# Performance work log

Measured on AMD Instinct MI355X. Metric: run time of the kernel, lower is better.

Reference implementation:

```python
import jax, jax.numpy as jnp
import numpy as np
import math

B, T, F, H, C = 512, 26, 2048, 1024, 22


def _lstm_cell(x_t, h, c, Wih, Whh, bih, bhh):
    # PyTorch gate order: i, f, g, o. Gates: [B, 4H]
    gates = x_t @ Wih.T + h @ Whh.T + bih + bhh
    i, f, g, o = jnp.split(gates, 4, axis=-1)
    c_new = jax.nn.sigmoid(f) * c + jax.nn.sigmoid(i) * jnp.tanh(g)
    h_new = jax.nn.sigmoid(o) * jnp.tanh(c_new)
    return h_new, c_new


def setup_inputs() -> dict:
    key = jax.random.key(0)
    ks = jax.random.split(key, 13)
    s_enc = 1.0 / math.sqrt(H)
    inp = {
        "x": jax.random.normal(ks[0], (B, T, F), jnp.float32),
        "enc_Wih": jax.random.normal(ks[1], (4 * H, F), jnp.float32) * s_enc,
        "enc_Whh": jax.random.normal(ks[2], (4 * H, H), jnp.float32) * s_enc,
        "enc_bih": jax.random.normal(ks[3], (4 * H,), jnp.float32) * s_enc,
        "enc_bhh": jax.random.normal(ks[4], (4 * H,), jnp.float32) * s_enc,
        "proj_W": jax.random.normal(ks[5], (H, H), jnp.float32) * s_enc,
        "proj_b": jax.random.normal(ks[6], (H,), jnp.float32) * s_enc,
        "dec_Wih": jax.random.normal(ks[7], (4 * H, H + F), jnp.float32) * s_enc,
        "dec_Whh": jax.random.normal(ks[8], (4 * H, H), jnp.float32) * s_enc,
        "dec_bih": jax.random.normal(ks[9], (4 * H,), jnp.float32) * s_enc,
        "dec_bhh": jax.random.normal(ks[10], (4 * H,), jnp.float32) * s_enc,
        "cls_W": jax.random.normal(ks[11], (C, H), jnp.float32) * s_enc,
        "cls_b": jax.random.normal(ks[12], (C,), jnp.float32) * s_enc,
    }
    return inp


def reference(x, enc_Wih, enc_Whh, enc_bih, enc_bhh, proj_W, proj_b,
              dec_Wih, dec_Whh, dec_bih, dec_bhh, cls_W, cls_b):
    # feature_extractor treated as identity (fusion_size == F)
    b, t, _ = x.shape
    h = x.shape[-1]  # noqa (F)

    # ---- Encoder LSTM over time (batch_first) ----
    def enc_step(carry, x_t):
        h_prev, c_prev = carry
        h_new, c_new = _lstm_cell(x_t, h_prev, c_prev, enc_Wih, enc_Whh, enc_bih, enc_bhh)
        return (h_new, c_new), h_new

    h0 = jnp.zeros((b, H), x.dtype)
    c0 = jnp.zeros((b, H), x.dtype)
    xs = jnp.swapaxes(x, 0, 1)  # [T, B, F]
    _, h_ts = jax.lax.scan(enc_step, (h0, c0), xs)  # [T, B, H]
    h_ts = jnp.swapaxes(h_ts, 0, 1)  # [B, T, H]

    proj_h_ts = h_ts @ proj_W.T + proj_b  # [B, T, H]
    inv_sqrt_h = 1.0 / math.sqrt(H)

    # ---- Decoder with per-step attention ----
    def dec_step(carry, x_t):
        dec_h, dec_c = carry
        # attention scores over encoder timesteps
        attn_logits = jnp.einsum('bh,bth->bt', dec_h, proj_h_ts) * inv_sqrt_h
        attn_w = jax.nn.softmax(attn_logits, axis=-1)
        attn = jnp.einsum('bt,bth->bh', attn_w, proj_h_ts)  # [B, H]
        inp_t = jnp.concatenate([x_t, attn], axis=1)  # [B, F+H]
        dec_h, dec_c = _lstm_cell(inp_t, dec_h, dec_c, dec_Wih, dec_Whh, dec_bih, dec_bhh)
        score = dec_h @ cls_W.T + cls_b  # [B, C]
        return (dec_h, dec_c), score

    _, scores = jax.lax.scan(dec_step, (h0, c0), xs)  # [T, B, C]
    return jnp.swapaxes(scores, 0, 1)  # [B, T, C]
```

## Files before the change

### kernel.cpp

```cpp
#include <hip/hip_runtime.h>

#define DB 512
#define DT 26
#define DF 2048
#define DH 1024
#define DG 4096
#define DC 22

typedef unsigned short u16;
typedef u16 u16x8 __attribute__((ext_vector_type(8)));
typedef __bf16 bf16x8 __attribute__((ext_vector_type(8)));
typedef float f32x4 __attribute__((ext_vector_type(4)));

__device__ __forceinline__ float sigm(float x) { return 1.f / (1.f + __expf(-x)); }

__device__ __forceinline__ u16 f2b(float v) {
  unsigned u = __float_as_uint(v);
  return (u16)((u + 0x7FFFu + ((u >> 16) & 1u)) >> 16);
}
__device__ __forceinline__ float b2f(u16 h) {
  return __uint_as_float(((unsigned)h) << 16);
}
__device__ __forceinline__ void store_b4(u16* __restrict__ d, size_t o, float4 v) {
  ushort4 s;
  s.x = f2b(v.x); s.y = f2b(v.y); s.z = f2b(v.z); s.w = f2b(v.w);
  *(ushort4*)(d + o) = s;
}

template <int OUTBF>
__global__ __launch_bounds__(256) void gemm_bt(
    const u16* __restrict__ A1, long lda1, int K1,
    const u16* __restrict__ A2, long lda2,
    const u16* __restrict__ B, long ldb, const float* __restrict__ bias,
    void* __restrict__ Cp, long ldc, int M, int N, int K)
{
  constexpr int LR = 72;
  __shared__ __align__(16) u16 sA[64 * LR];
  __shared__ __align__(16) u16 sB[128 * LR];
  const int tid = threadIdx.x, lane = tid & 63;
  const int wid = tid >> 6, wm = wid >> 1, wn = wid & 1;
  const int nbn = N >> 7;
  const int cpx = gridDim.x >> 3;
  const int swz = (blockIdx.x & 7) * cpx + (blockIdx.x >> 3);
  const int bm = swz / nbn, bn = swz % nbn;
  const size_t m0 = (size_t)bm << 6, n0 = (size_t)bn << 7;

  const int row = tid >> 3, c8 = tid & 7;
  u16x8 ra[2], rb[4];

  auto loadA = [&](int k0) {
    const u16* p; long lda; int kk;
    if (k0 < K1) { p = A1; lda = lda1; kk = k0; }
    else         { p = A2; lda = lda2; kk = k0 - K1; }
#pragma unroll
    for (int r = 0; r < 2; ++r)
      ra[r] = *(const u16x8*)(p + (m0 + row + r * 32) * (size_t)lda + (size_t)(kk + c8 * 8));
  };
  auto loadB = [&](int k0) {
#pragma unroll
    for (int r = 0; r < 4; ++r)
      rb[r] = *(const u16x8*)(B + (n0 + row + r * 32) * (size_t)ldb + (size_t)(k0 + c8 * 8));
  };
  loadA(0);
  loadB(0);

  f32x4 acc[2][4] = {};
  for (int k0 = 0; k0 < K; k0 += 64) {
    __syncthreads();
#pragma unroll
    for (int r = 0; r < 2; ++r) *(u16x8*)(sA + (row + r * 32) * LR + c8 * 8) = ra[r];
#pragma unroll
    for (int r = 0; r < 4; ++r) *(u16x8*)(sB + (row + r * 32) * LR + c8 * 8) = rb[r];
    __syncthreads();
    if (k0 + 64 < K) { loadA(k0 + 64); loadB(k0 + 64); }
#pragma unroll
    for (int ks = 0; ks < 2; ++ks) {
      const int ko = ks * 32 + (lane >> 4) * 8;
      bf16x8 af[2], bfr[4];
#pragma unroll
      for (int mi = 0; mi < 2; ++mi)
        af[mi] = *(const bf16x8*)(sA + ((wm << 5) + (mi << 4) + (lane & 15)) * LR + ko);
#pragma unroll
      for (int ni = 0; ni < 4; ++ni)
        bfr[ni] = *(const bf16x8*)(sB + ((wn << 6) + (ni << 4) + (lane & 15)) * LR + ko);
#pragma unroll
      for (int mi = 0; mi < 2; ++mi)
#pragma unroll
        for (int ni = 0; ni < 4; ++ni)
          acc[mi][ni] = __builtin_amdgcn_mfma_f32_16x16x32_bf16(af[mi], bfr[ni], acc[mi][ni], 0, 0, 0);
    }
  }

#pragma unroll
  for (int mi = 0; mi < 2; ++mi) {
    const int row0 = (wm << 5) + (mi << 4) + ((lane >> 4) << 2);
#pragma unroll
    for (int ni = 0; ni < 4; ++ni) {
      const size_t gn = n0 + (size_t)((wn << 6) + (ni << 4) + (lane & 15));
      const float bv = bias[gn];
#pragma unroll
      for (int r = 0; r < 4; ++r) {
        const size_t gm = m0 + (size_t)(row0 + r);
        const float v = acc[mi][ni][r] + bv;
        if (OUTBF) __builtin_nontemporal_store(f2b(v), (u16*)Cp + gm * (size_t)ldc + gn);
        else       __builtin_nontemporal_store(v, (float*)Cp + gm * (size_t)ldc + gn);
      }
    }
  }
}

template <int PHASES>
__global__ __launch_bounds__(512) void step_panel(
    const u16* __restrict__ A, long lda,
    const u16* __restrict__ W, long ldw,
    const u16* __restrict__ xg, long ldxg,
    float* __restrict__ cst, u16* __restrict__ hout, long ldh, long hoff,
    int first)
{
  constexpr int LRP = 1032;
  __shared__ __align__(16) u16 sB[64 * LRP];
  const int tid = threadIdx.x, lane = tid & 63, w = tid >> 6;
  const int cpx = gridDim.x >> 3;
  const int swz = (blockIdx.x & 7) * cpx + (blockIdx.x >> 3);
  const int nblk = swz >> 2, mg = swz & 3;
  const int n0 = nblk << 6;
  const int l15 = lane & 15, l4 = lane >> 4;
  const int arow = mg * 128 + (w << 4) + l15;
  const int kof = l4 * 8;

  f32x4 acc[4] = {};
#pragma unroll
  for (int ph = 0; ph < PHASES; ++ph) {
    if (ph) __syncthreads();
#pragma unroll
    for (int i = 0; i < 16; ++i) {
      const int c = i * 512 + tid;
      const int r = c >> 7, cc = c & 127;
      *(u16x8*)(sB + r * LRP + cc * 8) =
          *(const u16x8*)(W + (size_t)(n0 + r) * ldw + ph * 1024 + cc * 8);
    }
    __syncthreads();

    const u16* Ap = A + (size_t)arow * lda + ph * 1024 + kof;
    bf16x8 af = *(const bf16x8*)(Ap);
#pragma unroll 2
    for (int ko = 0; ko < 1024; ko += 32) {
      bf16x8 afn = af;
      if (ko + 32 < 1024) afn = *(const bf16x8*)(Ap + ko + 32);
      bf16x8 b0 = *(const bf16x8*)(sB + (l15)      * LRP + ko + kof);
      bf16x8 b1 = *(const bf16x8*)(sB + (16 + l15) * LRP + ko + kof);
      bf16x8 b2 = *(const bf16x8*)(sB + (32 + l15) * LRP + ko + kof);
      bf16x8 b3 = *(const bf16x8*)(sB + (48 + l15) * LRP + ko + kof);
      acc[0] = __builtin_amdgcn_mfma_f32_16x16x32_bf16(af, b0, acc[0], 0, 0, 0);
      acc[1] = __builtin_amdgcn_mfma_f32_16x16x32_bf16(af, b1, acc[1], 0, 0, 0);
      acc[2] = __builtin_amdgcn_mfma_f32_16x16x32_bf16(af, b2, acc[2], 0, 0, 0);
      acc[3] = __builtin_amdgcn_mfma_f32_16x16x32_bf16(af, b3, acc[3], 0, 0, 0);
      af = afn;
    }
  }

  const int hg = (nblk << 4) | l15;
  const int row0 = mg * 128 + (w << 4) + (l4 << 2);
#pragma unroll
  for (int r = 0; r < 4; ++r) {
    const int gm = row0 + r;
    const u16* xr = xg + (size_t)gm * ldxg + n0 + l15;
    const float gi = acc[0][r] + b2f(xr[0]);
    const float gf = acc[1][r] + b2f(xr[16]);
    const float gg = acc[2][r] + b2f(xr[32]);
    const float go = acc[3][r] + b2f(xr[48]);
    const size_t ch = ((size_t)gm << 10) + hg;
    const float cp = first ? 0.f : cst[ch];
    const float cn = sigm(gf) * cp + sigm(gi) * tanhf(gg);
    const float hn = sigm(go) * tanhf(cn);
    cst[ch] = cn;
    hout[(size_t)gm * ldh + hoff + hg] = f2b(hn);
  }
}

__global__ __launch_bounds__(256) void cvt4_kernel(const float* __restrict__ src,
    u16* __restrict__ dst, int n4) {
  for (int i = blockIdx.x * 256 + threadIdx.x; i < n4; i += gridDim.x * 256) {
    float4 v = *(const float4*)(src + (size_t)i * 4);
    store_b4(dst, (size_t)i * 4, v);
  }
}

__global__ __launch_bounds__(256) void pack_perm_kernel(const float* __restrict__ src,
    long ld_src, long scol, int cols4, u16* __restrict__ dst, long ld_dst, long dcol) {
  const int total = DG * cols4;
  for (int i = blockIdx.x * 256 + threadIdx.x; i < total; i += gridDim.x * 256) {
    const int np = i / cols4, c4 = i - np * cols4;
    const int g = (np >> 4) & 3, h = ((np >> 6) << 4) | (np & 15);
    const int n = g * 1024 + h;
    float4 v = *(const float4*)(src + (size_t)n * ld_src + scol + (size_t)c4 * 4);
    store_b4(dst, (size_t)np * ld_dst + dcol + (size_t)c4 * 4, v);
  }
}

__global__ void pack_bias_perm_kernel(const float* __restrict__ a,
    const float* __restrict__ b, float* __restrict__ o) {
  int np = blockIdx.x * 256 + threadIdx.x;
  if (np < DG) {
    const int g = (np >> 4) & 3, h = ((np >> 6) << 4) | (np & 15);
    const int n = g * 1024 + h;
    o[np] = a[n] + b[n];
  }
}

template <int DO_ATTN>
__global__ __launch_bounds__(256) void attn_cls_kernel(
    const u16* __restrict__ projH, const u16* __restrict__ Zr, u16* __restrict__ Zw,
    const float* __restrict__ clsW, const float* __restrict__ clsb,
    float* __restrict__ out, int do_cls, int tprev)
{
  const int b = blockIdx.x, tid = threadIdx.x, lane = tid & 63, wid = tid >> 6;
  __shared__ float redc[DC][4];
  __shared__ float red[DT][4];
  __shared__ float wgt[DT];

  ushort4 hz = *(const ushort4*)(Zr + ((size_t)b << 11) + 1024 + tid * 4);
  float4 hv = make_float4(b2f(hz.x), b2f(hz.y), b2f(hz.z), b2f(hz.w));

  if (do_cls) {
    float acc[DC];
#pragma unroll
    for (int c = 0; c < DC; ++c) {
      const float4 w = *(const float4*)(clsW + ((size_t)c << 10) + tid * 4);
      acc[c] = hv.x * w.x + hv.y * w.y + hv.z * w.z + hv.w * w.w;
    }
#pragma unroll
    for (int c = 0; c < DC; ++c) {
      float v = acc[c];
#pragma unroll
      for (int off = 32; off; off >>= 1) v += __shfl_xor(v, off);
      if (lane == 0) redc[c][wid] = v;
    }
  }

  if (DO_ATTN) {
    float ph[DT][4];
    float p[DT];
#pragma unroll
    for (int t = 0; t < DT; ++t) {
      ushort4 pv = *(const ushort4*)(projH + (((size_t)t * DB + b) << 10) + tid * 4);
      ph[t][0] = b2f(pv.x); ph[t][1] = b2f(pv.y); ph[t][2] = b2f(pv.z); ph[t][3] = b2f(pv.w);
      p[t] = hv.x * ph[t][0] + hv.y * ph[t][1] + hv.z * ph[t][2] + hv.w * ph[t][3];
    }
#pragma unroll
    for (int t = 0; t < DT; ++t) {
#pragma unroll
      for (int off = 32; off; off >>= 1) p[t] += __shfl_xor(p[t], off);
      if (lane == 0) red[t][wid] = p[t];
    }
    __syncthreads();
    if (tid == 0) {
      float lg[DT];
      float mx = -1e30f;
#pragma unroll
      for (int t = 0; t < DT; ++t) {
        lg[t] = (red[t][0] + red[t][1] + red[t][2] + red[t][3]) * 0.03125f;
        mx = fmaxf(mx, lg[t]);
      }
      float s = 0.f;
#pragma unroll
      for (int t = 0; t < DT; ++t) { lg[t] = __expf(lg[t] - mx); s += lg[t]; }
      float inv = 1.f / s;
#pragma unroll
      for (int t = 0; t < DT; ++t) wgt[t] = lg[t] * inv;
    }
    __syncthreads();
    float4 a = make_float4(0, 0, 0, 0);
#pragma unroll
    for (int t = 0; t < DT; ++t) {
      const float w = wgt[t];
      a.x += w * ph[t][0]; a.y += w * ph[t][1]; a.z += w * ph[t][2]; a.w += w * ph[t][3];
    }
    store_b4(Zw, ((size_t)b << 11) + tid * 4, a);
  }

  if (do_cls) {
    __syncthreads();
    if (tid < DC)
      out[((size_t)b * DT + tprev) * DC + tid] =
          redc[tid][0] + redc[tid][1] + redc[tid][2] + redc[tid][3] + clsb[tid];
  }
}

extern "C" void kernel_launch(void* const* d_in, const int* in_sizes, int n_in,
                              void* d_out, int out_size, void* d_ws, size_t ws_size,
                              hipStream_t stream) {
  const float* x    = (const float*)d_in[0];
  const float* eWih = (const float*)d_in[1];
  const float* eWhh = (const float*)d_in[2];
  const float* ebih = (const float*)d_in[3];
  const float* ebhh = (const float*)d_in[4];
  const float* pW   = (const float*)d_in[5];
  const float* pb   = (const float*)d_in[6];
  const float* dWih = (const float*)d_in[7];
  const float* dWhh = (const float*)d_in[8];
  const float* dbih = (const float*)d_in[9];
  const float* dbhh = (const float*)d_in[10];
  const float* clsW = (const float*)d_in[11];
  const float* clsb = (const float*)d_in[12];
  float* out = (float*)d_out;

  char* p = (char*)d_ws;
  auto alloc = [&](size_t bytes) -> void* {
    char* r = p; p += (bytes + 255) & ~(size_t)255; return (void*)r;
  };
  u16* Xb    = (u16*)alloc((size_t)DB * DT * DF * 2);
  u16* eWx   = (u16*)alloc((size_t)DG * 2048 * 2);
  u16* eWh   = (u16*)alloc((size_t)DG * 1024 * 2);
  u16* dWx   = (u16*)alloc((size_t)DG * 2048 * 2);
  u16* dWah  = (u16*)alloc((size_t)DG * 2048 * 2);
  u16* pWb   = (u16*)alloc((size_t)DH * DH * 2);
  u16* Hb    = (u16*)alloc((size_t)DT * DB * DH * 2);
  u16* encXg = (u16*)alloc((size_t)DB * DT * DG * 2);
  u16* decXg = (u16*)alloc((size_t)DB * DT * DG * 2);
  u16* Z0    = (u16*)alloc((size_t)DB * 2048 * 2);
  u16* Z1    = (u16*)alloc((size_t)DB * 2048 * 2);
  u16* Hz    = (u16*)alloc((size_t)DB * DH * 2);
  float* eCs = (float*)alloc((size_t)DB * DH * 4);
  float* dCs = (float*)alloc((size_t)DB * DH * 4);
  float* ebs = (float*)alloc(DG * 4);
  float* dbs = (float*)alloc(DG * 4);
  u16* projHb = Xb;

  cvt4_kernel<<<2048, 256, 0, stream>>>(x, Xb, (int)((size_t)DB * DT * DF / 4));
  pack_perm_kernel<<<2048, 256, 0, stream>>>(eWih, DF, 0, DF / 4, eWx, 2048, 0);
  pack_perm_kernel<<<2048, 256, 0, stream>>>(eWhh, DH, 0, DH / 4, eWh, 1024, 0);
  pack_perm_kernel<<<2048, 256, 0, stream>>>(dWih, 3072, 0, DF / 4, dWx, 2048, 0);
  pack_perm_kernel<<<2048, 256, 0, stream>>>(dWih, 3072, 2048, DH / 4, dWah, 2048, 0);
  pack_perm_kernel<<<2048, 256, 0, stream>>>(dWhh, DH, 0, DH / 4, dWah, 2048, 1024);
  cvt4_kernel<<<1024, 256, 0, stream>>>(pW, pWb, DH * DH / 4);
  pack_bias_perm_kernel<<<16, 256, 0, stream>>>(ebih, ebhh, ebs);
  pack_bias_perm_kernel<<<16, 256, 0, stream>>>(dbih, dbhh, dbs);
  hipMemsetAsync(Hz, 0, (size_t)DB * DH * 2, stream);
  hipMemsetAsync(Z0, 0, (size_t)DB * 2048 * 2, stream);

  gemm_bt<1><<<6656, 256, 0, stream>>>(
      Xb, DF, DF, Xb, DF, eWx, DF, ebs, encXg, DG, DB * DT, DG, DF);
  gemm_bt<1><<<6656, 256, 0, stream>>>(
      Xb, DF, DF, Xb, DF, dWx, DF, dbs, decXg, DG, DB * DT, DG, DF);

  for (int t = 0; t < DT; ++t) {
    step_panel<1><<<256, 512, 0, stream>>>(
        (t == 0) ? Hz : (Hb + (size_t)(t - 1) * DB * DH), DH,
        eWh, 1024,
        encXg + (size_t)t * DG, (long)DT * DG, eCs,
        Hb + (size_t)t * DB * DH, DH, 0, t == 0);
  }

  gemm_bt<1><<<1664, 256, 0, stream>>>(
      Hb, DH, DH, Hb, DH, pWb, DH, pb, projHb, DH, DT * DB, DH, DH);

  for (int t = 0; t < DT; ++t) {
    u16* Zc = (t & 1) ? Z1 : Z0;
    u16* Zn = (t & 1) ? Z0 : Z1;
    attn_cls_kernel<1><<<DB, 256, 0, stream>>>(
        projHb, Zc, Zc, clsW, clsb, out, t > 0, t - 1);
    step_panel<2><<<256, 512, 0, stream>>>(
        Zc, 2048, dWah, 2048,
        decXg + (size_t)t * DG, (long)DT * DG, dCs,
        Zn, 2048, 1024, t == 0);
  }
  attn_cls_kernel<0><<<DB, 256, 0, stream>>>(
      projHb, Z0, Z0, clsW, clsb, out, 1, DT - 1);
}
```

Measured before the change: 2.635 ms.

## Replace per-timestep launches with persistent encoder/decoder kernels using grid barriers

Encoder and decoder recurrences each become one persistent kernel of 256 blocks that loops over timesteps and synchronises through an atomic grid barrier, instead of launching 26 to 52 small kernels. Cell state now stays in registers rather than a global buffer, the encoder's recurrent weight panel stays resident in LDS for every step, and attention plus classifier work is folded into the decoder kernel. The GEMM tile order is also switched to M-major and its stores made ordinary instead of nontemporal. The cost is reliance on all 256 blocks being co-resident for the spin barrier, plus extra barrier latency per step.

```diff
diff --git a/kernel.cpp b/kernel.cpp
--- a/kernel.cpp
+++ b/kernel.cpp
@@ -6,6 +6,8 @@
 #define DH 1024
 #define DG 4096
 #define DC 22
+#define NBLK 256
+#define LRP 1040
 
 typedef unsigned short u16;
 typedef u16 u16x8 __attribute__((ext_vector_type(8)));
@@ -25,6 +27,24 @@
   ushort4 s;
   s.x = f2b(v.x); s.y = f2b(v.y); s.z = f2b(v.z); s.w = f2b(v.w);
   *(ushort4*)(d + o) = s;
+}
+
+__device__ __forceinline__ void gridbar(int* __restrict__ cnt, int* __restrict__ gen) {
+  __syncthreads();
+  if (threadIdx.x == 0) {
+    __threadfence();
+    int g = __hip_atomic_load(gen, __ATOMIC_RELAXED, __HIP_MEMORY_SCOPE_AGENT);
+    int old = __hip_atomic_fetch_add(cnt, 1, __ATOMIC_ACQ_REL, __HIP_MEMORY_SCOPE_AGENT);
+    if (old == NBLK - 1) {
+      __hip_atomic_store(cnt, 0, __ATOMIC_RELAXED, __HIP_MEMORY_SCOPE_AGENT);
+      __hip_atomic_store(gen, g + 1, __ATOMIC_RELEASE, __HIP_MEMORY_SCOPE_AGENT);
+    } else {
+      while (__hip_atomic_load(gen, __ATOMIC_ACQUIRE, __HIP_MEMORY_SCOPE_AGENT) == g)
+        __builtin_amdgcn_s_sleep(8);
+    }
+    __threadfence();
+  }
+  __syncthreads();
 }
 
 template <int OUTBF>
@@ -39,10 +59,10 @@
   __shared__ __align__(16) u16 sB[128 * LR];
   const int tid = threadIdx.x, lane = tid & 63;
   const int wid = tid >> 6, wm = wid >> 1, wn = wid & 1;
-  const int nbn = N >> 7;
+  const int nbm = M >> 6;
   const int cpx = gridDim.x >> 3;
   const int swz = (blockIdx.x & 7) * cpx + (blockIdx.x >> 3);
-  const int bm = swz / nbn, bn = swz % nbn;
+  const int bn = swz / nbm, bm = swz % nbm;
   const size_t m0 = (size_t)bm << 6, n0 = (size_t)bn << 7;
 
   const int row = tid >> 3, c8 = tid & 7;
@@ -102,79 +122,216 @@
       for (int r = 0; r < 4; ++r) {
         const size_t gm = m0 + (size_t)(row0 + r);
         const float v = acc[mi][ni][r] + bv;
-        if (OUTBF) __builtin_nontemporal_store(f2b(v), (u16*)Cp + gm * (size_t)ldc + gn);
-        else       __builtin_nontemporal_store(v, (float*)Cp + gm * (size_t)ldc + gn);
-      }
-    }
-  }
-}
-
-template <int PHASES>
-__global__ __launch_bounds__(512) void step_panel(
-    const u16* __restrict__ A, long lda,
-    const u16* __restrict__ W, long ldw,
-    const u16* __restrict__ xg, long ldxg,
-    float* __restrict__ cst, u16* __restrict__ hout, long ldh, long hoff,
-    int first)
+        if (OUTBF) ((u16*)Cp)[gm * (size_t)ldc + gn] = f2b(v);
+        else       ((float*)Cp)[gm * (size_t)ldc + gn] = v;
+      }
+    }
+  }
+}
+
+__global__ __launch_bounds__(512) void enc_persist(
+    const u16* __restrict__ W,
+    const u16* __restrict__ xg,
+    u16* __restrict__ H,
+    int* __restrict__ cnt, int* __restrict__ gen)
 {
-  constexpr int LRP = 1032;
   __shared__ __align__(16) u16 sB[64 * LRP];
   const int tid = threadIdx.x, lane = tid & 63, w = tid >> 6;
-  const int cpx = gridDim.x >> 3;
-  const int swz = (blockIdx.x & 7) * cpx + (blockIdx.x >> 3);
-  const int nblk = swz >> 2, mg = swz & 3;
+  const int nblk = blockIdx.x >> 2, mg = blockIdx.x & 3;
   const int n0 = nblk << 6;
   const int l15 = lane & 15, l4 = lane >> 4;
   const int arow = mg * 128 + (w << 4) + l15;
   const int kof = l4 * 8;
-
-  f32x4 acc[4] = {};
-#pragma unroll
-  for (int ph = 0; ph < PHASES; ++ph) {
-    if (ph) __syncthreads();
-#pragma unroll
-    for (int i = 0; i < 16; ++i) {
-      const int c = i * 512 + tid;
-      const int r = c >> 7, cc = c & 127;
-      *(u16x8*)(sB + r * LRP + cc * 8) =
-          *(const u16x8*)(W + (size_t)(n0 + r) * ldw + ph * 1024 + cc * 8);
-    }
-    __syncthreads();
-
-    const u16* Ap = A + (size_t)arow * lda + ph * 1024 + kof;
-    bf16x8 af = *(const bf16x8*)(Ap);
-#pragma unroll 2
-    for (int ko = 0; ko < 1024; ko += 32) {
-      bf16x8 afn = af;
-      if (ko + 32 < 1024) afn = *(const bf16x8*)(Ap + ko + 32);
-      bf16x8 b0 = *(const bf16x8*)(sB + (l15)      * LRP + ko + kof);
-      bf16x8 b1 = *(const bf16x8*)(sB + (16 + l15) * LRP + ko + kof);
-      bf16x8 b2 = *(const bf16x8*)(sB + (32 + l15) * LRP + ko + kof);
-      bf16x8 b3 = *(const bf16x8*)(sB + (48 + l15) * LRP + ko + kof);
-      acc[0] = __builtin_amdgcn_mfma_f32_16x16x32_bf16(af, b0, acc[0], 0, 0, 0);
-      acc[1] = __builtin_amdgcn_mfma_f32_16x16x32_bf16(af, b1, acc[1], 0, 0, 0);
-      acc[2] = __builtin_amdgcn_mfma_f32_16x16x32_bf16(af, b2, acc[2], 0, 0, 0);
-      acc[3] = __builtin_amdgcn_mfma_f32_16x16x32_bf16(af, b3, acc[3], 0, 0, 0);
-      af = afn;
-    }
-  }
-
   const int hg = (nblk << 4) | l15;
   const int row0 = mg * 128 + (w << 4) + (l4 << 2);
-#pragma unroll
-  for (int r = 0; r < 4; ++r) {
-    const int gm = row0 + r;
-    const u16* xr = xg + (size_t)gm * ldxg + n0 + l15;
-    const float gi = acc[0][r] + b2f(xr[0]);
-    const float gf = acc[1][r] + b2f(xr[16]);
-    const float gg = acc[2][r] + b2f(xr[32]);
-    const float go = acc[3][r] + b2f(xr[48]);
-    const size_t ch = ((size_t)gm << 10) + hg;
-    const float cp = first ? 0.f : cst[ch];
-    const float cn = sigm(gf) * cp + sigm(gi) * tanhf(gg);
-    const float hn = sigm(go) * tanhf(cn);
-    cst[ch] = cn;
-    hout[(size_t)gm * ldh + hoff + hg] = f2b(hn);
+
+#pragma unroll
+  for (int i = 0; i < 16; ++i) {
+    const int c = i * 512 + tid, r = c >> 7, cc = c & 127;
+    *(u16x8*)(sB + r * LRP + cc * 8) = *(const u16x8*)(W + (size_t)(n0 + r) * 1024 + cc * 8);
+  }
+  __syncthreads();
+
+  f32x4 creg = {0.f, 0.f, 0.f, 0.f};
+  for (int t = 0; t < DT; ++t) {
+    f32x4 acc[4] = {};
+    if (t > 0) {
+      const u16* Ap = H + (size_t)(t - 1) * DB * DH + (size_t)arow * DH + kof;
+      bf16x8 af = *(const bf16x8*)Ap;
+      for (int ko = 0; ko < 1024; ko += 32) {
+        bf16x8 afn = af;
+        if (ko + 32 < 1024) afn = *(const bf16x8*)(Ap + ko + 32);
+        bf16x8 b0 = *(const bf16x8*)(sB + (l15)      * LRP + ko + kof);
+        bf16x8 b1 = *(const bf16x8*)(sB + (16 + l15) * LRP + ko + kof);
+        bf16x8 b2 = *(const bf16x8*)(sB + (32 + l15) * LRP + ko + kof);
+        bf16x8 b3 = *(const bf16x8*)(sB + (48 + l15) * LRP + ko + kof);
+        acc[0] = __builtin_amdgcn_mfma_f32_16x16x32_bf16(af, b0, acc[0], 0, 0, 0);
+        acc[1] = __builtin_amdgcn_mfma_f32_16x16x32_bf16(af, b1, acc[1], 0, 0, 0);
+        acc[2] = __builtin_amdgcn_mfma_f32_16x16x32_bf16(af, b2, acc[2], 0, 0, 0);
+        acc[3] = __builtin_amdgcn_mfma_f32_16x16x32_bf16(af, b3, acc[3], 0, 0, 0);
+        af = afn;
+      }
+    }
+    u16* Hw = H + (size_t)t * DB * DH;
+#pragma unroll
+    for (int r = 0; r < 4; ++r) {
+      const int gm = row0 + r;
+      const u16* xr = xg + ((size_t)gm * DT + t) * DG + n0 + l15;
+      const float gi = acc[0][r] + b2f(xr[0]);
+      const float gf = acc[1][r] + b2f(xr[16]);
+      const float gg = acc[2][r] + b2f(xr[32]);
+      const float go = acc[3][r] + b2f(xr[48]);
+      const float cn = sigm(gf) * creg[r] + sigm(gi) * tanhf(gg);
+      creg[r] = cn;
+      Hw[(size_t)gm * DH + hg] = f2b(sigm(go) * tanhf(cn));
+    }
+    if (t < DT - 1) gridbar(cnt, gen);
+  }
+}
+
+__global__ __launch_bounds__(512) void dec_persist(
+    const u16* __restrict__ W,
+    const u16* __restrict__ xg,
+    const u16* __restrict__ projH,
+    u16* __restrict__ Z0, u16* __restrict__ Z1,
+    const float* __restrict__ clsW, const float* __restrict__ clsb,
+    float* __restrict__ out, int* __restrict__ cnt, int* __restrict__ gen)
+{
+  __shared__ __align__(16) u16 sB[64 * LRP];
+  __shared__ float red[2][DT][4];
+  __shared__ float redc[2][DC][4];
+  __shared__ float wgt[2][DT];
+  const int tid = threadIdx.x, lane = tid & 63, w = tid >> 6;
+  const int nblk = blockIdx.x >> 2, mg = blockIdx.x & 3;
+  const int n0 = nblk << 6;
+  const int l15 = lane & 15, l4 = lane >> 4;
+  const int arow = mg * 128 + (w << 4) + l15;
+  const int kof = l4 * 8;
+  const int hg = (nblk << 4) | l15;
+  const int row0 = mg * 128 + (w << 4) + (l4 << 2);
+  const int rr = tid >> 8, t4 = tid & 255, wv = (tid >> 6) & 3;
+  const int b = 2 * blockIdx.x + rr;
+
+  f32x4 creg = {0.f, 0.f, 0.f, 0.f};
+  for (int t = 0; t < DT; ++t) {
+    u16* Zin  = (t & 1) ? Z1 : Z0;
+    u16* Zout = (t & 1) ? Z0 : Z1;
+
+    ushort4 hz = *(const ushort4*)(Zin + ((size_t)b << 11) + 1024 + t4 * 4);
+    float4 hv = make_float4(b2f(hz.x), b2f(hz.y), b2f(hz.z), b2f(hz.w));
+    ushort4 ph[DT];
+    float pp[DT];
+#pragma unroll
+    for (int tt = 0; tt < DT; ++tt) {
+      ph[tt] = *(const ushort4*)(projH + (((size_t)tt * DB + b) << 10) + t4 * 4);
+      pp[tt] = hv.x * b2f(ph[tt].x) + hv.y * b2f(ph[tt].y) +
+               hv.z * b2f(ph[tt].z) + hv.w * b2f(ph[tt].w);
+    }
+#pragma unroll
+    for (int tt = 0; tt < DT; ++tt) {
+      float v = pp[tt];
+#pragma unroll
+      for (int off = 32; off; off >>= 1) v += __shfl_xor(v, off);
+      if (lane == 0) red[rr][tt][wv] = v;
+    }
+    if (t > 0) {
+#pragma unroll
+      for (int c = 0; c < DC; ++c) {
+        const float4 wc = *(const float4*)(clsW + ((size_t)c << 10) + t4 * 4);
+        float v = hv.x * wc.x + hv.y * wc.y + hv.z * wc.z + hv.w * wc.w;
+#pragma unroll
+        for (int off = 32; off; off >>= 1) v += __shfl_xor(v, off);
+        if (lane == 0) redc[rr][c][wv] = v;
+      }
+    }
+    __syncthreads();
+    if (t4 == 0) {
+      float lg[DT], mx = -1e30f;
+#pragma unroll
+      for (int tt = 0; tt < DT; ++tt) {
+        lg[tt] = (red[rr][tt][0] + red[rr][tt][1] + red[rr][tt][2] + red[rr][tt][3]) * 0.03125f;
+        mx = fmaxf(mx, lg[tt]);
+      }
+      float s = 0.f;
+#pragma unroll
+      for (int tt = 0; tt < DT; ++tt) { lg[tt] = __expf(lg[tt] - mx); s += lg[tt]; }
+      const float inv = 1.f / s;
+#pragma unroll
+      for (int tt = 0; tt < DT; ++tt) wgt[rr][tt] = lg[tt] * inv;
+    }
+    __syncthreads();
+    if (t > 0 && t4 < DC)
+      out[((size_t)b * DT + (t - 1)) * DC + t4] =
+          redc[rr][t4][0] + redc[rr][t4][1] + redc[rr][t4][2] + redc[rr][t4][3] + clsb[t4];
+    float4 a = make_float4(0, 0, 0, 0);
+#pragma unroll
+    for (int tt = 0; tt < DT; ++tt) {
+      const float wt = wgt[rr][tt];
+      a.x += wt * b2f(ph[tt].x); a.y += wt * b2f(ph[tt].y);
+      a.z += wt * b2f(ph[tt].z); a.w += wt * b2f(ph[tt].w);
+    }
+    store_b4(Zin, ((size_t)b << 11) + t4 * 4, a);
+    gridbar(cnt, gen);
+
+    f32x4 acc[4] = {};
+    for (int phx = 0; phx < 2; ++phx) {
+      if (phx == 1 && t == 0) break;
+      if (!(t == 1 && phx == 0)) {
+        if (phx) __syncthreads();
+#pragma unroll
+        for (int i = 0; i < 16; ++i) {
+          const int c = i * 512 + tid, r = c >> 7, cc = c & 127;
+          *(u16x8*)(sB + r * LRP + cc * 8) =
+              *(const u16x8*)(W + (size_t)(n0 + r) * 2048 + phx * 1024 + cc * 8);
+        }
+        __syncthreads();
+      }
+      const u16* Ap = Zin + (size_t)arow * 2048 + phx * 1024 + kof;
+      bf16x8 af = *(const bf16x8*)Ap;
+      for (int ko = 0; ko < 1024; ko += 32) {
+        bf16x8 afn = af;
+        if (ko + 32 < 1024) afn = *(const bf16x8*)(Ap + ko + 32);
+        bf16x8 b0 = *(const bf16x8*)(sB + (l15)      * LRP + ko + kof);
+        bf16x8 b1 = *(const bf16x8*)(sB + (16 + l15) * LRP + ko + kof);
+        bf16x8 b2 = *(const bf16x8*)(sB + (32 + l15) * LRP + ko + kof);
+        bf16x8 b3 = *(const bf16x8*)(sB + (48 + l15) * LRP + ko + kof);
+        acc[0] = __builtin_amdgcn_mfma_f32_16x16x32_bf16(af, b0, acc[0], 0, 0, 0);
+        acc[1] = __builtin_amdgcn_mfma_f32_16x16x32_bf16(af, b1, acc[1], 0, 0, 0);
+        acc[2] = __builtin_amdgcn_mfma_f32_16x16x32_bf16(af, b2, acc[2], 0, 0, 0);
+        acc[3] = __builtin_amdgcn_mfma_f32_16x16x32_bf16(af, b3, acc[3], 0, 0, 0);
+        af = afn;
+      }
+    }
+#pragma unroll
+    for (int r = 0; r < 4; ++r) {
+      const int gm = row0 + r;
+      const u16* xr = xg + ((size_t)gm * DT + t) * DG + n0 + l15;
+      const float gi = acc[0][r] + b2f(xr[0]);
+      const float gf = acc[1][r] + b2f(xr[16]);
+      const float gg = acc[2][r] + b2f(xr[32]);
+      const float go = acc[3][r] + b2f(xr[48]);
+      const float cn = sigm(gf) * creg[r] + sigm(gi) * tanhf(gg);
+      creg[r] = cn;
+      Zout[((size_t)gm << 11) + 1024 + hg] = f2b(sigm(go) * tanhf(cn));
+    }
+    gridbar(cnt, gen);
+  }
+
+  {
+    ushort4 hz = *(const ushort4*)(Z0 + ((size_t)b << 11) + 1024 + t4 * 4);
+    float4 hv = make_float4(b2f(hz.x), b2f(hz.y), b2f(hz.z), b2f(hz.w));
+#pragma unroll
+    for (int c = 0; c < DC; ++c) {
+      const float4 wc = *(const float4*)(clsW + ((size_t)c << 10) + t4 * 4);
+      float v = hv.x * wc.x + hv.y * wc.y + hv.z * wc.z + hv.w * wc.w;
+#pragma unroll
+      for (int off = 32; off; off >>= 1) v += __shfl_xor(v, off);
+      if (lane == 0) redc[rr][c][wv] = v;
+    }
+    __syncthreads();
+    if (t4 < DC)
+      out[((size_t)b * DT + (DT - 1)) * DC + t4] =
+          redc[rr][t4][0] + redc[rr][t4][1] + redc[rr][t4][2] + redc[rr][t4][3] + clsb[t4];
   }
 }
 
@@ -205,85 +362,6 @@
     const int g = (np >> 4) & 3, h = ((np >> 6) << 4) | (np & 15);
     const int n = g * 1024 + h;
     o[np] = a[n] + b[n];
-  }
-}
-
-template <int DO_ATTN>
-__global__ __launch_bounds__(256) void attn_cls_kernel(
-    const u16* __restrict__ projH, const u16* __restrict__ Zr, u16* __restrict__ Zw,
-    const float* __restrict__ clsW, const float* __restrict__ clsb,
-    float* __restrict__ out, int do_cls, int tprev)
-{
-  const int b = blockIdx.x, tid = threadIdx.x, lane = tid & 63, wid = tid >> 6;
-  __shared__ float redc[DC][4];
-  __shared__ float red[DT][4];
-  __shared__ float wgt[DT];
-
-  ushort4 hz = *(const ushort4*)(Zr + ((size_t)b << 11) + 1024 + tid * 4);
-  float4 hv = make_float4(b2f(hz.x), b2f(hz.y), b2f(hz.z), b2f(hz.w));
-
-  if (do_cls) {
-    float acc[DC];
-#pragma unroll
-    for (int c = 0; c < DC; ++c) {
-      const float4 w = *(const float4*)(clsW + ((size_t)c << 10) + tid * 4);
-      acc[c] = hv.x * w.x + hv.y * w.y + hv.z * w.z + hv.w * w.w;
-    }
-#pragma unroll
-    for (int c = 0; c < DC; ++c) {
-      float v = acc[c];
-#pragma unroll
-      for (int off = 32; off; off >>= 1) v += __shfl_xor(v, off);
-      if (lane == 0) redc[c][wid] = v;
-    }
-  }
-
-  if (DO_ATTN) {
-    float ph[DT][4];
-    float p[DT];
-#pragma unroll
-    for (int t = 0; t < DT; ++t) {
-      ushort4 pv = *(const ushort4*)(projH + (((size_t)t * DB + b) << 10) + tid * 4);
-      ph[t][0] = b2f(pv.x); ph[t][1] = b2f(pv.y); ph[t][2] = b2f(pv.z); ph[t][3] = b2f(pv.w);
-      p[t] = hv.x * ph[t][0] + hv.y * ph[t][1] + hv.z * ph[t][2] + hv.w * ph[t][3];
-    }
-#pragma unroll
-    for (int t = 0; t < DT; ++t) {
-#pragma unroll
-      for (int off = 32; off; off >>= 1) p[t] += __shfl_xor(p[t], off);
-      if (lane == 0) red[t][wid] = p[t];
-    }
-    __syncthreads();
-    if (tid == 0) {
-      float lg[DT];
-      float mx = -1e30f;
-#pragma unroll
-      for (int t = 0; t < DT; ++t) {
-        lg[t] = (red[t][0] + red[t][1] + red[t][2] + red[t][3]) * 0.03125f;
-        mx = fmaxf(mx, lg[t]);
-      }
-      float s = 0.f;
-#pragma unroll
-      for (int t = 0; t < DT; ++t) { lg[t] = __expf(lg[t] - mx); s += lg[t]; }
-      float inv = 1.f / s;
-#pragma unroll
-      for (int t = 0; t < DT; ++t) wgt[t] = lg[t] * inv;
-    }
-    __syncthreads();
-    float4 a = make_float4(0, 0, 0, 0);
-#pragma unroll
-    for (int t = 0; t < DT; ++t) {
-      const float w = wgt[t];
-      a.x += w * ph[t][0]; a.y += w * ph[t][1]; a.z += w * ph[t][2]; a.w += w * ph[t][3];
-    }
-    store_b4(Zw, ((size_t)b << 11) + tid * 4, a);
-  }
-
-  if (do_cls) {
-    __syncthreads();
-    if (tid < DC)
-      out[((size_t)b * DT + tprev) * DC + tid] =
-          redc[tid][0] + redc[tid][1] + redc[tid][2] + redc[tid][3] + clsb[tid];
   }
 }
 
@@ -320,13 +398,13 @@
   u16* decXg = (u16*)alloc((size_t)DB * DT * DG * 2);
   u16* Z0    = (u16*)alloc((size_t)DB * 2048 * 2);
   u16* Z1    = (u16*)alloc((size_t)DB * 2048 * 2);
-  u16* Hz    = (u16*)alloc((size_t)DB * DH * 2);
-  float* eCs = (float*)alloc((size_t)DB * DH * 4);
-  float* dCs = (float*)alloc((size_t)DB * DH * 4);
   float* ebs = (float*)alloc(DG * 4);
   float* dbs = (float*)alloc(DG * 4);
+  int* bar   = (int*)alloc(256);
   u16* projHb = Xb;
 
+  hipMemsetAsync(bar, 0, 256, stream);
+  hipMemsetAsync(Z0, 0, (size_t)DB * 2048 * 2, stream);
   cvt4_kernel<<<2048, 256, 0, stream>>>(x, Xb, (int)((size_t)DB * DT * DF / 4));
   pack_perm_kernel<<<2048, 256, 0, stream>>>(eWih, DF, 0, DF / 4, eWx, 2048, 0);
   pack_perm_kernel<<<2048, 256, 0, stream>>>(eWhh, DH, 0, DH / 4, eWh, 1024, 0);
@@ -336,35 +414,17 @@
   cvt4_kernel<<<1024, 256, 0, stream>>>(pW, pWb, DH * DH / 4);
   pack_bias_perm_kernel<<<16, 256, 0, stream>>>(ebih, ebhh, ebs);
   pack_bias_perm_kernel<<<16, 256, 0, stream>>>(dbih, dbhh, dbs);
-  hipMemsetAsync(Hz, 0, (size_t)DB * DH * 2, stream);
-  hipMemsetAsync(Z0, 0, (size_t)DB * 2048 * 2, stream);
 
   gemm_bt<1><<<6656, 256, 0, stream>>>(
       Xb, DF, DF, Xb, DF, eWx, DF, ebs, encXg, DG, DB * DT, DG, DF);
   gemm_bt<1><<<6656, 256, 0, stream>>>(
       Xb, DF, DF, Xb, DF, dWx, DF, dbs, decXg, DG, DB * DT, DG, DF);
 
-  for (int t = 0; t < DT; ++t) {
-    step_panel<1><<<256, 512, 0, stream>>>(
-        (t == 0) ? Hz : (Hb + (size_t)(t - 1) * DB * DH), DH,
-        eWh, 1024,
-        encXg + (size_t)t * DG, (long)DT * DG, eCs,
-        Hb + (size_t)t * DB * DH, DH, 0, t == 0);
-  }
+  enc_persist<<<NBLK, 512, 0, stream>>>(eWh, encXg, Hb, bar, bar + 64);
 
   gemm_bt<1><<<1664, 256, 0, stream>>>(
       Hb, DH, DH, Hb, DH, pWb, DH, pb, projHb, DH, DT * DB, DH, DH);
 
-  for (int t = 0; t < DT; ++t) {
-    u16* Zc = (t & 1) ? Z1 : Z0;
-    u16* Zn = (t & 1) ? Z0 : Z1;
-    attn_cls_kernel<1><<<DB, 256, 0, stream>>>(
-        projHb, Zc, Zc, clsW, clsb, out, t > 0, t - 1);
-    step_panel<2><<<256, 512, 0, stream>>>(
-        Zc, 2048, dWah, 2048,
-        decXg + (size_t)t * DG, (long)DT * DG, dCs,
-        Zn, 2048, 1024, t == 0);
-  }
-  attn_cls_kernel<0><<<DB, 256, 0, stream>>>(
-      projHb, Z0, Z0, clsW, clsb, out, 1, DT - 1);
-}
+  dec_persist<<<NBLK, 512, 0, stream>>>(
+      dWah, decXg, projHb, Z0, Z1, clsW, clsb, out, bar, bar + 64);
+}
```

After: 4.172 ms. +58.3%, slower.
